# Performance work log

Hardware: AMD Instinct MI355X
Metric: run time of the kernel (lower is better)

## Reference

```python
import jax, jax.numpy as jnp
import numpy as np

HEADS = 4
DIM_HEAD = 32
DIM = 128
HIDDEN = HEADS * DIM_HEAD  # 128
SCALE = DIM_HEAD ** -0.5


def setup_inputs() -> dict:
    key = jax.random.key(0)
    ks = jax.random.split(key, 7)
    b, c, h, w = 4, DIM, 256, 256
    x = jax.random.normal(ks[0], (b, c, h, w), dtype=jnp.float32)
    context = jax.random.normal(ks[1], (b, c, h, w), dtype=jnp.float32)
    # conv1x1 weights stored as [out, in] matrices
    s_in = 1.0 / np.sqrt(DIM)
    Wq = jax.random.uniform(ks[2], (HIDDEN, DIM), jnp.float32, -s_in, s_in)
    Wk = jax.random.uniform(ks[3], (HIDDEN, DIM), jnp.float32, -s_in, s_in)
    Wv = jax.random.uniform(ks[4], (HIDDEN, DIM), jnp.float32, -s_in, s_in)
    s_h = 1.0 / np.sqrt(HIDDEN)
    Wo = jax.random.uniform(ks[5], (DIM, HIDDEN), jnp.float32, -s_h, s_h)
    bo = jax.random.uniform(ks[6], (DIM,), jnp.float32, -s_h, s_h)
    return {"x": x, "context": context, "Wq": Wq, "Wk": Wk, "Wv": Wv, "Wo": Wo, "bo": bo}


def reference(x, context, Wq, Wk, Wv, Wo, bo):
    b, c, h, w = x.shape
    n = h * w
    xf = x.reshape(b, c, n)         # flatten spatial
    cf = context.reshape(b, c, n)
    # conv1x1 projections == channel matmuls
    q = jnp.einsum('oc,bcn->bon', Wq, xf).reshape(b, HEADS, DIM_HEAD, n)
    k = jnp.einsum('oc,bcn->bon', Wk, cf).reshape(b, HEADS, DIM_HEAD, n)
    v = jnp.einsum('oc,bcn->bon', Wv, cf).reshape(b, HEADS, DIM_HEAD, n)
    q = q * SCALE
    k = jax.nn.softmax(k, axis=-1)  # softmax over spatial positions
    ctx = jnp.einsum('bhdn,bhen->bhde', k, v)   # [b,h,d,e] small d_head x d_head
    out = jnp.einsum('bhde,bhdn->bhen', ctx, q)  # [b,h,e,n]
    out = out.reshape(b, HIDDEN, n)
    out = jnp.einsum('oc,bcn->bon', Wo, out) + bo[None, :, None]
    return out.reshape(b, c, h, w)
```

## Files before the change

kernel.cpp:

```cpp
#include <hip/hip_runtime.h>
#include <cstdint>
#include <cstddef>

typedef __bf16 bf16x8 __attribute__((ext_vector_type(8)));
typedef float f32x4 __attribute__((ext_vector_type(4)));
typedef float f32x16 __attribute__((ext_vector_type(16)));
typedef unsigned int u32x2 __attribute__((ext_vector_type(2)));
typedef unsigned int u32x4 __attribute__((ext_vector_type(4)));

#define MFMA16(a, b, c) __builtin_amdgcn_mfma_f32_16x16x32_bf16((a), (b), (c), 0, 0, 0)
#define MFMA32(a, b, c) __builtin_amdgcn_mfma_f32_32x32x16_bf16((a), (b), (c), 0, 0, 0)

#define BAR() asm volatile("s_waitcnt lgkmcnt(0)\n\ts_barrier" ::: "memory")

static constexpr int CD = 128;
static constexpr int NTOK = 65536;
static constexpr float F_SCALE = 0.17677669529663688f;
static constexpr float F_LOG2E = 1.4426950408889634f;
static constexpr int PART = 4224;
static constexpr int NPARTS = 128;

__device__ __forceinline__ unsigned pk2(float a, float b) {
  unsigned short ua = __builtin_bit_cast(unsigned short, (__bf16)a);
  unsigned short ub = __builtin_bit_cast(unsigned short, (__bf16)b);
  return (unsigned)ua | ((unsigned)ub << 16);
}

__device__ __forceinline__ f32x16 z16() {
  f32x16 v;
#pragma unroll
  for (int i = 0; i < 16; ++i) v[i] = 0.f;
  return v;
}

struct Grp { f32x4 M[4]; };

__device__ __forceinline__ Grp load_grp(const float* src, int lane) {
  Grp g;
  const float* p = src + (size_t)((lane >> 4) * 4) * NTOK + (lane & 15) * 4;
#pragma unroll
  for (int v = 0; v < 4; ++v) g.M[v] = *(const f32x4*)(p + (size_t)v * NTOK);
  return g;
}

__device__ __forceinline__ void pack_grp(const Grp& g, char* T2, int cqBase, int lane) {
  int cq = cqBase + (lane >> 4);
  int nq = lane & 15;
#pragma unroll
  for (int j = 0; j < 4; ++j) {
    int n = nq * 4 + j;
    *(u32x2*)(T2 + n * 256 + ((cq * 8) ^ ((n & 15) << 4))) =
        u32x2{pk2(g.M[0][j], g.M[1][j]), pk2(g.M[2][j], g.M[3][j])};
  }
}

__global__ __launch_bounds__(256) __attribute__((amdgpu_waves_per_eu(2)))
void k1_ctx(const float* __restrict__ ctx_in, const float* __restrict__ Wk,
            const float* __restrict__ Wv, float* __restrict__ S_part) {
  __shared__ char smem[32 * 1024];
  const int tid = threadIdx.x;
  const int lane = tid & 63;
  const int w = tid >> 6;
  const int l31 = lane & 31;
  const int l2 = lane >> 5;
  const int b = blockIdx.x >> 7;
  const int cb = blockIdx.x & 127;

  bf16x8 WfK[8], WfV[8];
#pragma unroll
  for (int ks = 0; ks < 8; ++ks) {
    const float* pK = Wk + (size_t)(w * 32 + l31) * CD + ks * 16 + l2 * 8;
    const float* pV = Wv + (size_t)(w * 32 + l31) * CD + ks * 16 + l2 * 8;
#pragma unroll
    for (int e = 0; e < 8; ++e) {
      WfK[ks][e] = (__bf16)(pK[e] * F_LOG2E);
      WfV[ks][e] = (__bf16)pV[e];
    }
  }

  f32x16 Sacc = z16();
  float zacc = 0.f;

  const float* srcA = ctx_in + (size_t)b * CD * NTOK + (size_t)(w * 32) * NTOK + cb * 512;
  const float* srcB = srcA + (size_t)16 * NTOK;

  Grp fa = load_grp(srcA, lane), fb = load_grp(srcB, lane);
#pragma unroll
  for (int s = 0; s < 8; ++s) {
    char* T2 = smem + (s & 1) * 16384;
    pack_grp(fa, T2, w * 8, lane);
    pack_grp(fb, T2, w * 8 + 4, lane);
    if (s < 7) {
      fa = load_grp(srcA + (s + 1) * 64, lane);
      fb = load_grp(srcB + (s + 1) * 64, lane);
    }
    BAR();

    unsigned pe[2][4][2], pv[2][4][2];
#pragma unroll
    for (int t = 0; t < 2; ++t) {
      f32x16 aK = z16(), aV = z16();
#pragma unroll
      for (int ks = 0; ks < 8; ++ks) {
        bf16x8 At = *(const bf16x8*)(T2 + (t * 32 + l31) * 256 +
                                     ((ks * 32 + l2 * 16) ^ ((l31 & 15) << 4)));
        aK = MFMA32(At, WfK[ks], aK);
        aV = MFMA32(At, WfV[ks], aV);
      }
#pragma unroll
      for (int q = 0; q < 4; ++q) {
        float e0 = __builtin_exp2f(aK[4 * q + 0]);
        float e1 = __builtin_exp2f(aK[4 * q + 1]);
        float e2 = __builtin_exp2f(aK[4 * q + 2]);
        float e3 = __builtin_exp2f(aK[4 * q + 3]);
        zacc += (e0 + e1) + (e2 + e3);
        pe[t][q][0] = pk2(e0, e1);
        pe[t][q][1] = pk2(e2, e3);
        pv[t][q][0] = pk2(aV[4 * q + 0], aV[4 * q + 1]);
        pv[t][q][1] = pk2(aV[4 * q + 2], aV[4 * q + 3]);
      }
    }

#pragma unroll
    for (int nw = 0; nw < 4; ++nw) {
      const int t = nw >> 1, w2 = nw & 1;
      unsigned ea0 = pe[t][2 * w2][0], eb0 = pe[t][2 * w2 + 1][0];
      unsigned ea1 = pe[t][2 * w2][1], eb1 = pe[t][2 * w2 + 1][1];
      asm("v_permlane32_swap_b32 %0, %1" : "+v"(ea0), "+v"(eb0));
      asm("v_permlane32_swap_b32 %0, %1" : "+v"(ea1), "+v"(eb1));
      unsigned va0 = pv[t][2 * w2][0], vb0 = pv[t][2 * w2 + 1][0];
      unsigned va1 = pv[t][2 * w2][1], vb1 = pv[t][2 * w2 + 1][1];
      asm("v_permlane32_swap_b32 %0, %1" : "+v"(va0), "+v"(vb0));
      asm("v_permlane32_swap_b32 %0, %1" : "+v"(va1), "+v"(vb1));
      bf16x8 Ea = __builtin_bit_cast(bf16x8, u32x4{ea0, ea1, eb0, eb1});
      bf16x8 Vb = __builtin_bit_cast(bf16x8, u32x4{va0, va1, vb0, vb1});
      Sacc = MFMA32(Ea, Vb, Sacc);
    }
  }

  float* outp = S_part + (size_t)blockIdx.x * PART;
#pragma unroll
  for (int q = 0; q < 4; ++q) {
    f32x4 v{Sacc[4 * q + 0], Sacc[4 * q + 1], Sacc[4 * q + 2], Sacc[4 * q + 3]};
    *(f32x4*)(outp + w * 1024 + lane * 16 + q * 4) = v;
  }
  zacc += __shfl_xor(zacc, 32, 64);
  if (l2 == 0) outp[4096 + w * 32 + l31] = zacc;
}

__global__ void k2a_reduce(const float* __restrict__ S_part, float* __restrict__ S_red,
                           float* __restrict__ Z_red) {
  int bid = blockIdx.x;
  int b = bid / 33, bs = bid % 33;
  int tid = threadIdx.x;
  __shared__ float red[256];
  int e_loc = tid & 127, half = tid >> 7;
  const float* base =
      S_part + (size_t)b * NPARTS * PART + (bs < 32 ? bs * 128 + e_loc : 4096 + e_loc);
  float sum = 0.f;
  int h = NPARTS >> 1;
  for (int p = half * h; p < half * h + h; ++p) sum += base[(size_t)p * PART];
  red[tid] = sum;
  __syncthreads();
  if (tid < 128) {
    float v = red[tid] + red[tid + 128];
    if (bs < 32)
      S_red[b * 4096 + bs * 128 + tid] = v;
    else
      Z_red[b * 128 + tid] = v;
  }
}

__global__ void k2b_weff(const float* __restrict__ S_red, const float* __restrict__ Z_red,
                         const float* __restrict__ Wq, const float* __restrict__ Wo,
                         float* __restrict__ W_eff) {
  int b = blockIdx.x >> 3, og = blockIdx.x & 7;
  int tid = threadIdx.x;
  __shared__ float ctx_lds[4096];
  __shared__ float T_lds[16 * 128];
  for (int i = tid * 16; i < tid * 16 + 16; ++i) {
    int h = i >> 10, d = (i >> 5) & 31, e = i & 31;
    int fl = h * 1024 + ((e + ((d >> 2) & 1) * 32) << 4) + (d & 3) + ((d >> 3) << 2);
    ctx_lds[i] = S_red[b * 4096 + fl] / Z_red[b * 128 + h * 32 + d];
  }
  __syncthreads();
  {
    int o_loc = tid >> 4, hd0 = (tid & 15) * 8;
    int o = og * 16 + o_loc;
    for (int j = 0; j < 8; ++j) {
      int hd = hd0 + j, h = hd >> 5, d = hd & 31;
      const float* wo = Wo + o * 128 + h * 32;
      const float* cx = ctx_lds + h * 1024 + d * 32;
      float acc = 0.f;
      for (int e = 0; e < 32; ++e) acc += wo[e] * cx[e];
      T_lds[o_loc * 128 + hd] = acc;
    }
  }
  __syncthreads();
  {
    int o_loc = tid >> 4, c0 = (tid & 15) * 8;
    float acc[8] = {};
    const float* Trow = T_lds + o_loc * 128;
    for (int hd = 0; hd < 128; ++hd) {
      float tv = Trow[hd];
      const float* wq = Wq + hd * 128 + c0;
#pragma unroll
      for (int j = 0; j < 8; ++j) acc[j] += tv * wq[j];
    }
    float* op = W_eff + b * 16384 + (og * 16 + o_loc) * 128 + c0;
#pragma unroll
    for (int j = 0; j < 8; ++j) op[j] = F_SCALE * acc[j];
  }
}

__global__ __launch_bounds__(256, 4) void k3_out(const float* __restrict__ x,
                                                 const float* __restrict__ W_eff,
                                                 const float* __restrict__ bo,
                                                 float* __restrict__ out) {
  __shared__ char smem[32 * 1024];
  const int tid = threadIdx.x;
  const int lane = tid & 63;
  const int w = tid >> 6;
  const int l15 = lane & 15;
  const int lg = lane >> 4;
  const int b = blockIdx.x >> 8;
  const int cb = blockIdx.x & 255;

  bf16x8 Wf[2][4];
#pragma unroll
  for (int m = 0; m < 2; ++m) {
    int o = w * 32 + m * 16 + l15;
#pragma unroll
    for (int ks = 0; ks < 4; ++ks) {
      const float* p = W_eff + b * 16384 + o * 128 + ks * 32 + lg * 8;
#pragma unroll
      for (int e = 0; e < 8; ++e) Wf[m][ks][e] = (__bf16)p[e];
    }
  }
  float bof[2] = {bo[w * 32 + l15], bo[w * 32 + 16 + l15]};

  const float* srcA = x + (size_t)b * CD * NTOK + (size_t)(w * 32) * NTOK + cb * 256;
  const float* srcB = srcA + (size_t)16 * NTOK;
  float* dst = out + (size_t)b * CD * NTOK + cb * 256;

  Grp fa = load_grp(srcA, lane), fb = load_grp(srcB, lane);
#pragma unroll
  for (int s = 0; s < 4; ++s) {
    char* T2 = smem + (s & 1) * 16384;
    pack_grp(fa, T2, w * 8, lane);
    pack_grp(fb, T2, w * 8 + 4, lane);
    if (s < 3) {
      fa = load_grp(srcA + (s + 1) * 64, lane);
      fb = load_grp(srcB + (s + 1) * 64, lane);
    }
    BAR();

#pragma unroll
    for (int t = 0; t < 4; ++t) {
      f32x4 acc[2];
      acc[0] = f32x4{0.f, 0.f, 0.f, 0.f};
      acc[1] = f32x4{0.f, 0.f, 0.f, 0.f};
#pragma unroll
      for (int ks = 0; ks < 4; ++ks) {
        bf16x8 At = *(const bf16x8*)(T2 + (t * 16 + l15) * 256 +
                                     ((ks * 64 + lg * 16) ^ (l15 << 4)));
#pragma unroll
        for (int m = 0; m < 2; ++m) acc[m] = MFMA16(At, Wf[m][ks], acc[m]);
      }
#pragma unroll
      for (int m = 0; m < 2; ++m) {
        int o = w * 32 + m * 16 + l15;
        f32x4 v = acc[m];
        v[0] += bof[m]; v[1] += bof[m]; v[2] += bof[m]; v[3] += bof[m];
        *(f32x4*)(dst + (size_t)o * NTOK + s * 64 + t * 16 + lg * 4) = v;
      }
    }
  }
}

extern "C" void kernel_launch(void* const* d_in, const int* in_sizes, int n_in,
                              void* d_out, int out_size, void* d_ws, size_t ws_size,
                              hipStream_t stream) {
  const float* x = (const float*)d_in[0];
  const float* ctxg = (const float*)d_in[1];
  const float* Wq = (const float*)d_in[2];
  const float* Wk = (const float*)d_in[3];
  const float* Wv = (const float*)d_in[4];
  const float* Wo = (const float*)d_in[5];
  const float* bo = (const float*)d_in[6];
  float* out = (float*)d_out;

  float* ws = (float*)d_ws;
  float* S_part = ws;
  float* S_red = ws + (size_t)512 * PART;
  float* Z_red = S_red + 16384;
  float* W_eff = Z_red + 512;

  k1_ctx<<<dim3(512), dim3(256), 0, stream>>>(ctxg, Wk, Wv, S_part);
  k2a_reduce<<<dim3(132), dim3(256), 0, stream>>>(S_part, S_red, Z_red);
  k2b_weff<<<dim3(32), dim3(256), 0, stream>>>(S_red, Z_red, Wq, Wo, W_eff);
  k3_out<<<dim3(1024), dim3(256), 0, stream>>>(x, W_eff, bo, out);
}
```

Measured before the change: 155.3 us.

## Halve k3 token tile, double grid, and refine LDS swizzle to cut bank conflicts

The output kernel now processes 128 tokens per block instead of 256, using a new 32-token-wide load/pack path and 16 KB of LDS. This doubles the grid to 2048 blocks and raises the occupancy hint to 5 blocks per EU. The LDS XOR swizzle in both k1 and k3 now also mixes in the high bits of the row index, to reduce bank conflicts on packing and MFMA operand reads. The trade-off is shorter per-block pipelines, narrower 128-byte global row segments, and more per-block overhead such as reloading the weights.

```diff
diff --git a/kernel.cpp b/kernel.cpp
--- a/kernel.cpp
+++ b/kernel.cpp
@@ -49,8 +49,33 @@
 #pragma unroll
   for (int j = 0; j < 4; ++j) {
     int n = nq * 4 + j;
-    *(u32x2*)(T2 + n * 256 + ((cq * 8) ^ ((n & 15) << 4))) =
+    *(u32x2*)(T2 + n * 256 + ((cq * 8) ^ ((((n & 15) ^ (n >> 4))) << 4))) =
         u32x2{pk2(g.M[0][j], g.M[1][j]), pk2(g.M[2][j], g.M[3][j])};
+  }
+}
+
+struct Grp32 { f32x4 M[4]; };
+
+__device__ __forceinline__ Grp32 load_grp32(const float* src, int lane) {
+  Grp32 g;
+  int q = (lane >> 3) & 7;
+  const float* p = src + (size_t)(2 * q) * NTOK + (lane & 7) * 4;
+  g.M[0] = *(const f32x4*)p;
+  g.M[1] = *(const f32x4*)(p + NTOK);
+  g.M[2] = *(const f32x4*)(p + (size_t)16 * NTOK);
+  g.M[3] = *(const f32x4*)(p + (size_t)17 * NTOK);
+  return g;
+}
+
+__device__ __forceinline__ void pack_grp32(const Grp32& g, char* T2, int cpBase, int lane) {
+  int q = (lane >> 3) & 7;
+  int a = lane & 7;
+#pragma unroll
+  for (int j = 0; j < 4; ++j) {
+    int n = a * 4 + j;
+    int sw = (((n & 15) ^ (n >> 4)) << 4);
+    *(unsigned*)(T2 + n * 256 + (((cpBase + q) * 4) ^ sw)) = pk2(g.M[0][j], g.M[1][j]);
+    *(unsigned*)(T2 + n * 256 + (((cpBase + 8 + q) * 4) ^ sw)) = pk2(g.M[2][j], g.M[3][j]);
   }
 }
 
@@ -102,8 +127,9 @@
       f32x16 aK = z16(), aV = z16();
 #pragma unroll
       for (int ks = 0; ks < 8; ++ks) {
-        bf16x8 At = *(const bf16x8*)(T2 + (t * 32 + l31) * 256 +
-                                     ((ks * 32 + l2 * 16) ^ ((l31 & 15) << 4)));
+        bf16x8 At = *(const bf16x8*)(
+            T2 + (t * 32 + l31) * 256 +
+            ((ks * 32 + l2 * 16) ^ (((l31 & 15) ^ (2 * t + (l31 >> 4))) << 4)));
         aK = MFMA32(At, WfK[ks], aK);
         aV = MFMA32(At, WfV[ks], aV);
       }
@@ -213,18 +239,18 @@
   }
 }
 
-__global__ __launch_bounds__(256, 4) void k3_out(const float* __restrict__ x,
+__global__ __launch_bounds__(256, 5) void k3_out(const float* __restrict__ x,
                                                  const float* __restrict__ W_eff,
                                                  const float* __restrict__ bo,
                                                  float* __restrict__ out) {
-  __shared__ char smem[32 * 1024];
+  __shared__ char smem[16 * 1024];
   const int tid = threadIdx.x;
   const int lane = tid & 63;
   const int w = tid >> 6;
   const int l15 = lane & 15;
   const int lg = lane >> 4;
-  const int b = blockIdx.x >> 8;
-  const int cb = blockIdx.x & 255;
+  const int b = blockIdx.x >> 9;
+  const int cb = blockIdx.x & 511;
 
   bf16x8 Wf[2][4];
 #pragma unroll
@@ -239,31 +265,26 @@
   }
   float bof[2] = {bo[w * 32 + l15], bo[w * 32 + 16 + l15]};
 
-  const float* srcA = x + (size_t)b * CD * NTOK + (size_t)(w * 32) * NTOK + cb * 256;
-  const float* srcB = srcA + (size_t)16 * NTOK;
-  float* dst = out + (size_t)b * CD * NTOK + cb * 256;
-
-  Grp fa = load_grp(srcA, lane), fb = load_grp(srcB, lane);
+  const float* src = x + (size_t)b * CD * NTOK + (size_t)(w * 32) * NTOK + cb * 128;
+  float* dst = out + (size_t)b * CD * NTOK + cb * 128;
+
+  Grp32 f = load_grp32(src, lane);
 #pragma unroll
   for (int s = 0; s < 4; ++s) {
-    char* T2 = smem + (s & 1) * 16384;
-    pack_grp(fa, T2, w * 8, lane);
-    pack_grp(fb, T2, w * 8 + 4, lane);
-    if (s < 3) {
-      fa = load_grp(srcA + (s + 1) * 64, lane);
-      fb = load_grp(srcB + (s + 1) * 64, lane);
-    }
+    char* T2 = smem + (s & 1) * 8192;
+    pack_grp32(f, T2, w * 16, lane);
+    if (s < 3) f = load_grp32(src + (s + 1) * 32, lane);
     BAR();
 
 #pragma unroll
-    for (int t = 0; t < 4; ++t) {
+    for (int t = 0; t < 2; ++t) {
       f32x4 acc[2];
       acc[0] = f32x4{0.f, 0.f, 0.f, 0.f};
       acc[1] = f32x4{0.f, 0.f, 0.f, 0.f};
 #pragma unroll
       for (int ks = 0; ks < 4; ++ks) {
         bf16x8 At = *(const bf16x8*)(T2 + (t * 16 + l15) * 256 +
-                                     ((ks * 64 + lg * 16) ^ (l15 << 4)));
+                                     ((ks * 64 + lg * 16) ^ ((l15 ^ t) << 4)));
 #pragma unroll
         for (int m = 0; m < 2; ++m) acc[m] = MFMA16(At, Wf[m][ks], acc[m]);
       }
@@ -272,7 +293,7 @@
         int o = w * 32 + m * 16 + l15;
         f32x4 v = acc[m];
         v[0] += bof[m]; v[1] += bof[m]; v[2] += bof[m]; v[3] += bof[m];
-        *(f32x4*)(dst + (size_t)o * NTOK + s * 64 + t * 16 + lg * 4) = v;
+        *(f32x4*)(dst + (size_t)o * NTOK + s * 32 + t * 16 + lg * 4) = v;
       }
     }
   }
@@ -299,5 +320,5 @@
   k1_ctx<<<dim3(512), dim3(256), 0, stream>>>(ctxg, Wk, Wv, S_part);
   k2a_reduce<<<dim3(132), dim3(256), 0, stream>>>(S_part, S_red, Z_red);
   k2b_weff<<<dim3(32), dim3(256), 0, stream>>>(S_red, Z_red, Wq, Wo, W_eff);
-  k3_out<<<dim3(1024), dim3(256), 0, stream>>>(x, W_eff, bo, out);
-}
+  k3_out<<<dim3(2048), dim3(256), 0, stream>>>(x, W_eff, bo, out);
+}
```

Measured after the change: 160.6 us. +3.5%, slower.

## Widen k3 token chunks to 128 with single-buffered LDS and wider swizzle

Applied to the files above, without the earlier changes.

The output kernel now loads 128 tokens per step in two steps instead of 64 tokens in four double-buffered steps. Each lane reads 32 contiguous-lane f32x4 rows, giving 512-byte coalesced global reads per channel row, and the channel interleave is absorbed by permuting the weight fragment elements. The LDS XOR swizzle gains a row-block term to avoid bank conflicts over 128 rows, and the same swizzle is applied in k1. The trade-off is that prefetch overlap is lost: there is a barrier after compute and registers hold 16 f32x4 at once, which may reduce occupancy.

```diff
diff --git a/kernel.cpp b/kernel.cpp
--- a/kernel.cpp
+++ b/kernel.cpp
@@ -49,7 +49,7 @@
 #pragma unroll
   for (int j = 0; j < 4; ++j) {
     int n = nq * 4 + j;
-    *(u32x2*)(T2 + n * 256 + ((cq * 8) ^ ((n & 15) << 4))) =
+    *(u32x2*)(T2 + n * 256 + ((cq * 8) ^ ((((n & 15) ^ (n >> 4))) << 4))) =
         u32x2{pk2(g.M[0][j], g.M[1][j]), pk2(g.M[2][j], g.M[3][j])};
   }
 }
@@ -102,8 +102,9 @@
       f32x16 aK = z16(), aV = z16();
 #pragma unroll
       for (int ks = 0; ks < 8; ++ks) {
-        bf16x8 At = *(const bf16x8*)(T2 + (t * 32 + l31) * 256 +
-                                     ((ks * 32 + l2 * 16) ^ ((l31 & 15) << 4)));
+        bf16x8 At = *(const bf16x8*)(
+            T2 + (t * 32 + l31) * 256 +
+            ((ks * 32 + l2 * 16) ^ (((l31 & 15) ^ (2 * t + (l31 >> 4))) << 4)));
         aK = MFMA32(At, WfK[ks], aK);
         aV = MFMA32(At, WfV[ks], aV);
       }
@@ -217,15 +218,19 @@
                                                  const float* __restrict__ W_eff,
                                                  const float* __restrict__ bo,
                                                  float* __restrict__ out) {
-  __shared__ char smem[32 * 1024];
+  __shared__ char T2[32 * 1024];
   const int tid = threadIdx.x;
   const int lane = tid & 63;
   const int w = tid >> 6;
   const int l15 = lane & 15;
   const int lg = lane >> 4;
+  const int l31 = lane & 31;
+  const int h = lane >> 5;
   const int b = blockIdx.x >> 8;
   const int cb = blockIdx.x & 255;
 
+  constexpr int perm[8] = {0, 2, 4, 6, 1, 3, 5, 7};
+
   bf16x8 Wf[2][4];
 #pragma unroll
   for (int m = 0; m < 2; ++m) {
@@ -234,36 +239,45 @@
     for (int ks = 0; ks < 4; ++ks) {
       const float* p = W_eff + b * 16384 + o * 128 + ks * 32 + lg * 8;
 #pragma unroll
-      for (int e = 0; e < 8; ++e) Wf[m][ks][e] = (__bf16)p[e];
+      for (int e = 0; e < 8; ++e) Wf[m][ks][e] = (__bf16)p[perm[e]];
     }
   }
   float bof[2] = {bo[w * 32 + l15], bo[w * 32 + 16 + l15]};
 
-  const float* srcA = x + (size_t)b * CD * NTOK + (size_t)(w * 32) * NTOK + cb * 256;
-  const float* srcB = srcA + (size_t)16 * NTOK;
+  const float* src = x + (size_t)b * CD * NTOK + (size_t)(w * 32) * NTOK + cb * 256;
   float* dst = out + (size_t)b * CD * NTOK + cb * 256;
 
-  Grp fa = load_grp(srcA, lane), fb = load_grp(srcB, lane);
-#pragma unroll
-  for (int s = 0; s < 4; ++s) {
-    char* T2 = smem + (s & 1) * 16384;
-    pack_grp(fa, T2, w * 8, lane);
-    pack_grp(fb, T2, w * 8 + 4, lane);
-    if (s < 3) {
-      fa = load_grp(srcA + (s + 1) * 64, lane);
-      fb = load_grp(srcB + (s + 1) * 64, lane);
-    }
+#pragma unroll
+  for (int s = 0; s < 2; ++s) {
+    f32x4 M[16];
+#pragma unroll
+    for (int g = 0; g < 4; ++g)
+#pragma unroll
+      for (int i = 0; i < 4; ++i)
+        M[g * 4 + i] =
+            *(const f32x4*)(src + (size_t)(g * 8 + 2 * i + h) * NTOK + s * 128 + l31 * 4);
+
+#pragma unroll
+    for (int g = 0; g < 4; ++g)
+#pragma unroll
+      for (int j = 0; j < 4; ++j) {
+        int n = l31 * 4 + j;
+        int nib = (n & 15) ^ (n >> 4);
+        *(u32x2*)(T2 + n * 256 + (((w * 4 + g) * 16 + h * 8) ^ (nib << 4))) =
+            u32x2{pk2(M[g * 4 + 0][j], M[g * 4 + 1][j]),
+                  pk2(M[g * 4 + 2][j], M[g * 4 + 3][j])};
+      }
     BAR();
 
 #pragma unroll
-    for (int t = 0; t < 4; ++t) {
+    for (int t = 0; t < 8; ++t) {
       f32x4 acc[2];
       acc[0] = f32x4{0.f, 0.f, 0.f, 0.f};
       acc[1] = f32x4{0.f, 0.f, 0.f, 0.f};
 #pragma unroll
       for (int ks = 0; ks < 4; ++ks) {
         bf16x8 At = *(const bf16x8*)(T2 + (t * 16 + l15) * 256 +
-                                     ((ks * 64 + lg * 16) ^ (l15 << 4)));
+                                     ((ks * 64 + lg * 16) ^ ((l15 ^ t) << 4)));
 #pragma unroll
         for (int m = 0; m < 2; ++m) acc[m] = MFMA16(At, Wf[m][ks], acc[m]);
       }
@@ -272,9 +286,10 @@
         int o = w * 32 + m * 16 + l15;
         f32x4 v = acc[m];
         v[0] += bof[m]; v[1] += bof[m]; v[2] += bof[m]; v[3] += bof[m];
-        *(f32x4*)(dst + (size_t)o * NTOK + s * 64 + t * 16 + lg * 4) = v;
-      }
-    }
+        *(f32x4*)(dst + (size_t)o * NTOK + s * 128 + t * 16 + lg * 4) = v;
+      }
+    }
+    BAR();
   }
 }
 
```

Result: slower. 198.6 us (+27.9%).
